# Performance work log

Measured on AMD Instinct MI355X. Metric: run time of the kernel, lower is better.

The kernel has to match this reference:

```python
import jax, jax.numpy as jnp
import numpy as np
from jax.experimental.ode import odeint

# Physical constants from sfr.__init__
L0 = 0.1      # rest length per segment
D = 0.0075    # tendon offset
DS = 0.005    # arclength step
A_EXT_MAX = 0.04           # max extension used when generating actions
L_MAX = L0 + A_EXT_MAX     # 0.14 -> fixed integration horizon
T = int(round(L_MAX / DS)) + 1  # 29 points: arange(0, L_MAX + DS, DS)
N_SEG = 3
BATCH = 16384


def _ode_fn(y, t):
    # y: [B, 14] = (r:3, R:9 row-major, ux, uy); constant-curvature Cosserat rod
    ux, uy = y[:, 12], y[:, 13]
    R = y[:, 3:12].reshape(-1, 3, 3)
    dr = R[:, :, 2]                      # R @ e3 = third column of R
    z = jnp.zeros_like(ux)
    u_hat = jnp.stack([
        jnp.stack([z, z, uy], axis=-1),
        jnp.stack([z, z, -ux], axis=-1),
        jnp.stack([-uy, ux, z], axis=-1),
    ], axis=-2)                          # [B, 3, 3]
    dR = jnp.einsum('bij,bjk->bik', R, u_hat)
    dz = jnp.zeros((y.shape[0], 2), y.dtype)  # u is constant along s
    return jnp.concatenate([dr, dR.reshape(-1, 9), dz], axis=1)


def setup_inputs() -> dict:
    key = jax.random.key(0)
    k1, k2 = jax.random.split(key)
    ext = jax.random.uniform(k1, (BATCH, N_SEG), dtype=jnp.float32) * A_EXT_MAX
    bend = (jax.random.uniform(k2, (BATCH, N_SEG, 2), dtype=jnp.float32) - 0.5) * 0.02
    actions = jnp.concatenate([ext[:, :, None], bend], axis=-1).reshape(BATCH, 9)
    return {"actions": actions}


def reference(actions):
    B = actions.shape[0]
    t_eval = jnp.arange(T, dtype=jnp.float32) * DS
    # y0 = (r=0, R=I, ux=uy=0)
    y0_base = jnp.concatenate([jnp.zeros(3, jnp.float32),
                               jnp.eye(3, dtype=jnp.float32).reshape(9),
                               jnp.zeros(2, jnp.float32)])
    y0 = jnp.tile(y0_base[None, :], (B, 1))
    row_idx = jnp.arange(T, dtype=jnp.int32)[:, None]  # [T, 1]
    sol_parts = []
    for n in range(N_SEG):
        a = actions[:, 3 * n:3 * n + 3]
        l = L0 + a[:, 0]
        ux = a[:, 2] / (-(l * D))
        uy = a[:, 1] / (l * D)
        y0 = y0.at[:, 12].set(ux).at[:, 13].set(uy)
        sol_b = odeint(_ode_fn, y0, t_eval, rtol=1e-5, atol=1e-7)  # [T, B, 14]
        # hold trajectory constant past each rod's own length (vectorized mask)
        lengths = (l / DS).astype(jnp.int32)                       # [B]
        t_idx = jnp.minimum(row_idx, lengths[None, :])             # [T, B]
        sol_m = jnp.take_along_axis(sol_b, t_idx[:, :, None], axis=0)
        sol_parts.append(sol_m)
        y0 = sol_m[-1]
    return jnp.concatenate(sol_parts, axis=0)  # [3*T, B, 14]
```

## Files before the change

### kernel.cpp

```cpp
#include <hip/hip_runtime.h>


namespace {

constexpr float kL0 = 0.1f;
constexpr float kD  = 0.0075f;
constexpr float kDS = 0.005f;
constexpr int   kT    = 29;
constexpr int   kNSeg = 3;

__device__ __forceinline__ void exp_and_p(float ux, float uy, float s,
                                          float E[9], float p[3]) {
    float th2   = ux * ux + uy * uy;
    float theta = sqrtf(th2);
    float A, Bv, c;
    if (theta < 1e-5f) {
        A  = s;
        Bv = 0.5f * s * s;
        c  = 1.0f;
    } else {
        float phi = s * theta;
        float sh, ch;
        sincosf(0.5f * phi, &sh, &ch);
        float si  = 2.0f * sh * ch;
        float sh2 = 2.0f * sh * sh;
        A  = si / theta;
        Bv = sh2 / th2;
        c  = 1.0f - sh2;
    }
    float Aux = A * ux, Auy = A * uy;
    E[0] = 1.0f - Bv * uy * uy;
    E[1] = Bv * ux * uy;
    E[2] = Auy;
    E[3] = E[1];
    E[4] = 1.0f - Bv * ux * ux;
    E[5] = -Aux;
    E[6] = -Auy;
    E[7] = Aux;
    E[8] = c;
    p[0] = Bv * uy;
    p[1] = -Bv * ux;
    p[2] = A;
}

__device__ __forceinline__ void seg_state(const float* __restrict__ actions,
                                          int b, int m, int t,
                                          float r[3], float R[9],
                                          float& ux, float& uy) {
    const float a0 = actions[(size_t)b * 9 + 3 * m + 0];
    const float a1 = actions[(size_t)b * 9 + 3 * m + 1];
    const float a2 = actions[(size_t)b * 9 + 3 * m + 2];
    float l  = kL0 + a0;
    float md = l * kD;
    ux = a2 / (-md);
    uy = a1 / md;
    int kmax = (int)(l / kDS);
    int tc = t < kmax ? t : kmax;
    float s = (float)tc * kDS;

    float E[9], p[3];
    exp_and_p(ux, uy, s, E, p);

    float nr[3], NR[9];
#pragma unroll
    for (int i = 0; i < 3; ++i) {
        nr[i] = r[i] + R[3 * i + 0] * p[0] + R[3 * i + 1] * p[1] + R[3 * i + 2] * p[2];
#pragma unroll
        for (int j = 0; j < 3; ++j) {
            NR[3 * i + j] = R[3 * i + 0] * E[j]
                          + R[3 * i + 1] * E[3 + j]
                          + R[3 * i + 2] * E[6 + j];
        }
    }
#pragma unroll
    for (int i = 0; i < 3; ++i) r[i] = nr[i];
#pragma unroll
    for (int i = 0; i < 9; ++i) R[i] = NR[i];
}

__global__ __launch_bounds__(256) void rollout(const float* __restrict__ actions,
                                               float* __restrict__ out, int B) {
    int b = blockIdx.x * blockDim.x + threadIdx.x;
    if (b >= B) return;
    int row = blockIdx.y;
    int n = row / kT;
    int t = row - n * kT;

    float r[3] = {0.f, 0.f, 0.f};
    float R[9] = {1.f, 0.f, 0.f, 0.f, 1.f, 0.f, 0.f, 0.f, 1.f};
    float ux, uy;

    if (n >= 1) seg_state(actions, b, 0, kT, r, R, ux, uy);
    if (n >= 2) seg_state(actions, b, 1, kT, r, R, ux, uy);
    seg_state(actions, b, n, t, r, R, ux, uy);

    float o[14];
#pragma unroll
    for (int i = 0; i < 3; ++i) {
        o[i] = r[i];
#pragma unroll
        for (int j = 0; j < 3; ++j) o[3 + 3 * i + j] = R[3 * i + j];
    }
    o[12] = ux;
    o[13] = uy;

    size_t base = ((size_t)row * (size_t)B + (size_t)b) * 14;
    float2* o2 = reinterpret_cast<float2*>(out + base);
#pragma unroll
    for (int i = 0; i < 7; ++i) o2[i] = make_float2(o[2 * i], o[2 * i + 1]);
}

}

extern "C" void kernel_launch(void* const* d_in, const int* in_sizes, int n_in,
                              void* d_out, int out_size, void* d_ws, size_t ws_size,
                              hipStream_t stream) {
    const float* actions = (const float*)d_in[0];
    float* out = (float*)d_out;
    int B = in_sizes[0] / 9;
    dim3 block(256);
    dim3 grid((B + 255) / 256, kNSeg * kT);
    rollout<<<grid, block, 0, stream>>>(actions, out, B);
}
```

Measured before the change: 101.5 us.

## Stage output through shared memory for coalesced float4 stores and use fast intrinsics

Each thread writes its 14-float state into shared memory, and the block then writes its contiguous output chunk with coalesced float4 stores instead of per-thread strided float2 stores. The sincos and divisions are also replaced with hardware fast-math intrinsics (__sincosf, rcp). This adds a block barrier and 14 KB of LDS per block and slightly reduces precision. Removing the bounds check assumes B is a multiple of 256.

```diff
diff --git a/kernel.cpp b/kernel.cpp
--- a/kernel.cpp
+++ b/kernel.cpp
@@ -8,6 +8,10 @@
 constexpr float kDS = 0.005f;
 constexpr int   kT    = 29;
 constexpr int   kNSeg = 3;
+
+__device__ __forceinline__ float fast_rcp(float x) {
+    return __builtin_amdgcn_rcpf(x);
+}
 
 __device__ __forceinline__ void exp_and_p(float ux, float uy, float s,
                                           float E[9], float p[3]) {
@@ -21,11 +25,12 @@
     } else {
         float phi = s * theta;
         float sh, ch;
-        sincosf(0.5f * phi, &sh, &ch);
+        __sincosf(0.5f * phi, &sh, &ch);
         float si  = 2.0f * sh * ch;
         float sh2 = 2.0f * sh * sh;
-        A  = si / theta;
-        Bv = sh2 / th2;
+        float rth = fast_rcp(theta);
+        A  = si * rth;
+        Bv = sh2 * rth * rth;
         c  = 1.0f - sh2;
     }
     float Aux = A * ux, Auy = A * uy;
@@ -80,8 +85,9 @@
 
 __global__ __launch_bounds__(256) void rollout(const float* __restrict__ actions,
                                                float* __restrict__ out, int B) {
+    __shared__ float smem[256 * 14];
+
     int b = blockIdx.x * blockDim.x + threadIdx.x;
-    if (b >= B) return;
     int row = blockIdx.y;
     int n = row / kT;
     int t = row - n * kT;
@@ -94,20 +100,26 @@
     if (n >= 2) seg_state(actions, b, 1, kT, r, R, ux, uy);
     seg_state(actions, b, n, t, r, R, ux, uy);
 
-    float o[14];
+    float* my = &smem[threadIdx.x * 14];
+    my[0] = r[0];  my[1] = r[1];  my[2] = r[2];
 #pragma unroll
-    for (int i = 0; i < 3; ++i) {
-        o[i] = r[i];
+    for (int i = 0; i < 9; ++i) my[3 + i] = R[i];
+    my[12] = ux;
+    my[13] = uy;
+    __syncthreads();
+
+    size_t blockbase = ((size_t)row * (size_t)B + (size_t)blockIdx.x * 256) * 14;
+    float4* o4 = reinterpret_cast<float4*>(out + blockbase);
+    const float4* s4 = reinterpret_cast<const float4*>(smem);
 #pragma unroll
-        for (int j = 0; j < 3; ++j) o[3 + 3 * i + j] = R[3 * i + j];
+    for (int k = 0; k < 3; ++k) {
+        int q = k * 256 + threadIdx.x;
+        o4[q] = s4[q];
     }
-    o[12] = ux;
-    o[13] = uy;
-
-    size_t base = ((size_t)row * (size_t)B + (size_t)b) * 14;
-    float2* o2 = reinterpret_cast<float2*>(out + base);
-#pragma unroll
-    for (int i = 0; i < 7; ++i) o2[i] = make_float2(o[2 * i], o[2 * i + 1]);
+    if (threadIdx.x < 128) {
+        int q = 768 + threadIdx.x;
+        o4[q] = s4[q];
+    }
 }
 
 }
```

Result: faster. 89.04 us (-12.2%).
